# Kernel optimization log

Hardware: AMD Instinct MI355X
Metric: run time of the kernel (lower is better)

The kernel has to match this reference:

```python
import jax, jax.numpy as jnp
import numpy as np

D = 256      # hidden_dim / d_model
NH = 8       # num_heads
HD = D // NH # head_dim = 32
FF = 2048    # dim_feedforward
L = 2        # num_transformer_layers
CIN = 512
NC = 80      # num_classes
NA = 3       # num_anchors
EPS = 1e-5


def _ln(x, s, b):
    m = jnp.mean(x, axis=-1, keepdims=True)
    v = jnp.mean(jnp.square(x - m), axis=-1, keepdims=True)
    return (x - m) * jax.lax.rsqrt(v + EPS) * s + b


def setup_inputs() -> dict:
    key = jax.random.key(0)
    ks = iter(jax.random.split(key, 64))
    def g(shape, scale=0.02):
        return (jax.random.normal(next(ks), shape, dtype=jnp.float32) * scale)
    inp = {
        "x": jax.random.normal(next(ks), (4, CIN, 40, 40), dtype=jnp.float32),
        "conv_w": g((CIN, D)), "conv_b": jnp.zeros((D,), jnp.float32),
        "pos": jax.random.normal(next(ks), (1, D, 1, 1), dtype=jnp.float32),
        # stacked per-layer params [L, ...], weights stored as [in, out]
        "qw": g((L, D, D)), "qb": jnp.zeros((L, D)),
        "kw": g((L, D, D)), "kb": jnp.zeros((L, D)),
        "vw": g((L, D, D)), "vb": jnp.zeros((L, D)),
        "pw": g((L, D, D)), "pb": jnp.zeros((L, D)),
        "ln1s": jnp.ones((L, D)), "ln1b": jnp.zeros((L, D)),
        "ln2s": jnp.ones((L, D)), "ln2b": jnp.zeros((L, D)),
        "f1w": g((L, D, FF)), "f1b": jnp.zeros((L, FF)),
        "f2w": g((L, FF, D)), "f2b": jnp.zeros((L, D)),
        "cls_w1": g((D, D)), "cls_b1": jnp.zeros((D,)),
        "cls_w2": g((D, NA * NC)), "cls_b2": jnp.zeros((NA * NC,)),
        "box_w1": g((D, D)), "box_b1": jnp.zeros((D,)),
        "box_w2": g((D, NA * 4)), "box_b2": jnp.zeros((NA * 4,)),
        "obj_w1": g((D, D)), "obj_b1": jnp.zeros((D,)),
        "obj_w2": g((D, NA)), "obj_b2": jnp.zeros((NA,)),
    }
    return inp


def reference(x, conv_w, conv_b, pos, qw, qb, kw, kb, vw, vb, pw, pb,
              ln1s, ln1b, ln2s, ln2b, f1w, f1b, f2w, f2b,
              cls_w1, cls_b1, cls_w2, cls_b2,
              box_w1, box_b1, box_w2, box_b2,
              obj_w1, obj_b1, obj_w2, obj_b2):
    B, C, H, W = x.shape
    # 1x1 conv projection + positional encoding (broadcast scalar-per-channel)
    h = jnp.einsum('bchw,cd->bdhw', x, conv_w) + conv_b[None, :, None, None]
    h = h + pos  # broadcasts over B,H,W
    # flatten to sequence [B, N, D]
    N = H * W
    h = jnp.transpose(h.reshape(B, D, N), (0, 2, 1))

    scale = 1.0 / np.sqrt(HD)
    for i in range(L):
        # pre-norm MHSA
        y = _ln(h, ln1s[i], ln1b[i])
        q = (y @ qw[i] + qb[i]).reshape(B, N, NH, HD)
        k = (y @ kw[i] + kb[i]).reshape(B, N, NH, HD)
        v = (y @ vw[i] + vb[i]).reshape(B, N, NH, HD)
        scores = jnp.einsum('bnhd,bmhd->bhnm', q, k) * scale
        attn = jax.nn.softmax(scores, axis=-1)
        o = jnp.einsum('bhnm,bmhd->bnhd', attn, v).reshape(B, N, D)
        h = h + (o @ pw[i] + pb[i])
        # pre-norm FFN
        y = _ln(h, ln2s[i], ln2b[i])
        h = h + (jax.nn.relu(y @ f1w[i] + f1b[i]) @ f2w[i] + f2b[i])

    # prediction heads
    cls = jax.nn.relu(h @ cls_w1 + cls_b1) @ cls_w2 + cls_b2   # [B,N,NA*NC]
    box = jax.nn.relu(h @ box_w1 + box_b1) @ box_w2 + box_b2   # [B,N,NA*4]
    obj = jax.nn.relu(h @ obj_w1 + obj_b1) @ obj_w2 + obj_b2   # [B,N,NA]

    cls = jnp.transpose(cls.reshape(B, H, W, NA, NC), (0, 3, 1, 2, 4))
    box = jnp.transpose(box.reshape(B, H, W, NA, 4), (0, 3, 1, 2, 4))
    obj = jnp.transpose(obj.reshape(B, H, W, NA), (0, 3, 1, 2))
    return cls, box, obj
```

## Files before the change

kernel.cpp:

```cpp
#include <hip/hip_runtime.h>
#include <math.h>

#define BB   4
#define CIN  512
#define DD   256
#define NP   1600
#define TT   (BB*NP)
#define FF   2048
#define NHH  8
#define HDD  32
#define NA   3
#define NC   80

typedef __attribute__((ext_vector_type(8))) short bf16x8_t;
typedef __attribute__((ext_vector_type(4))) float f32x4_t;
typedef __attribute__((ext_vector_type(16))) float f32x16_t;

static __device__ __forceinline__ ushort f2bf(float f) {
    unsigned int u = __float_as_uint(f);
    u += 0x7FFF + ((u >> 16) & 1);
    return (ushort)(u >> 16);
}
static __device__ __forceinline__ float bf2f(ushort u) {
    return __uint_as_float((unsigned int)u << 16);
}
static __device__ __forceinline__ unsigned int cvt_pk_bf16(float lo, float hi) {
    unsigned int r;
    asm("v_cvt_pk_bf16_f32 %0, %1, %2" : "=v"(r) : "v"(lo), "v"(hi));
    return r;
}
static __device__ __forceinline__ void swap32(unsigned int& a, unsigned int& b) {
    asm("v_permlane32_swap_b32 %0, %1" : "+v"(a), "+v"(b));
}
static __device__ __forceinline__ bf16x8_t pack4(unsigned int a, unsigned int b,
                                                 unsigned int c, unsigned int d) {
    union { uint4 u; bf16x8_t v; } t;
    t.u = make_uint4(a, b, c, d);
    return t.v;
}

struct WDesc { const float* src; ushort* dst; int R; int C; int ntiles; float scale; };
struct WPrep { WDesc d[16]; };

__global__ __launch_bounds__(256) void wprep_kernel(WPrep p) {
    __shared__ float tile[32][33];
    int t = blockIdx.x;
    int i = 0;
    while (t >= p.d[i].ntiles) { t -= p.d[i].ntiles; i++; }
    const float* src = p.d[i].src;
    ushort* dst = p.d[i].dst;
    int R = p.d[i].R, C = p.d[i].C;
    float sc = p.d[i].scale;
    int tC = C >> 5;
    int r0 = (t / tC) * 32, c0 = (t % tC) * 32;
    int tx = threadIdx.x, ty = threadIdx.y;
    #pragma unroll
    for (int j = 0; j < 32; j += 8)
        tile[ty + j][tx] = src[(size_t)(r0 + ty + j) * C + (c0 + tx)];
    __syncthreads();
    #pragma unroll
    for (int j = 0; j < 32; j += 8)
        dst[(size_t)(c0 + ty + j) * R + (r0 + tx)] = f2bf(tile[tx][ty + j] * sc);
}

__global__ __launch_bounds__(256) void head2_wprep_kernel(
        const float* __restrict__ cls_w2, const float* __restrict__ box_w2,
        const float* __restrict__ obj_w2, ushort* __restrict__ dst)
{
    int nrow = blockIdx.x;
    int k = threadIdx.x;
    float v = 0.f;
    if (nrow < 240)                      v = cls_w2[k * 240 + nrow];
    else if (nrow >= 256 && nrow < 268)  v = box_w2[k * 12 + (nrow - 256)];
    else if (nrow >= 320 && nrow < 323)  v = obj_w2[k * 3 + (nrow - 320)];
    dst[(size_t)nrow * 256 + k] = f2bf(v);
}

__global__ void transpose_x_kernel(const float* __restrict__ x, ushort* __restrict__ xT) {
    __shared__ float tile[32][33];
    int b  = blockIdx.z;
    int c0 = blockIdx.x * 32;
    int n0 = blockIdx.y * 32;
    int tx = threadIdx.x, ty = threadIdx.y;
    #pragma unroll
    for (int j = 0; j < 32; j += 8) {
        tile[ty + j][tx] = x[b * CIN * NP + (c0 + ty + j) * NP + (n0 + tx)];
    }
    __syncthreads();
    #pragma unroll
    for (int j = 0; j < 32; j += 8) {
        xT[(size_t)(b * NP + n0 + ty + j) * CIN + (c0 + tx)] = f2bf(tile[tx][ty + j]);
    }
}

#define GEMM_CORE_LDA(A_, Bt_, K_, LDA_)                                         \
    __shared__ ushort As[64][72];                                                \
    __shared__ ushort Bs[64][72];                                                \
    int tid  = threadIdx.x;                                                      \
    int lane = tid & 63, wid = tid >> 6;                                         \
    int wm = wid >> 1, wn = wid & 1;                                             \
    int m0 = blockIdx.y * 64, n0 = blockIdx.x * 64;                              \
    int ln31 = lane & 31, lg = lane >> 5;                                        \
    int srow = tid >> 2;                                                         \
    int scol = (tid & 3) * 16;                                                   \
    const ushort* ag = (A_)  + (size_t)(m0 + srow) * (LDA_) + scol;              \
    const ushort* bg = (Bt_) + (size_t)(n0 + srow) * (K_) + scol;                \
    f32x16_t acc = {};                                                           \
    for (int k0 = 0; k0 < (K_); k0 += 64) {                                      \
        uint4 av0 = *(const uint4*)(ag + k0);                                    \
        uint4 av1 = *(const uint4*)(ag + k0 + 8);                                \
        uint4 bv0 = *(const uint4*)(bg + k0);                                    \
        uint4 bv1 = *(const uint4*)(bg + k0 + 8);                                \
        *(uint4*)&As[srow][scol]     = av0;                                      \
        *(uint4*)&As[srow][scol + 8] = av1;                                      \
        *(uint4*)&Bs[srow][scol]     = bv0;                                      \
        *(uint4*)&Bs[srow][scol + 8] = bv1;                                      \
        __syncthreads();                                                         \
        _Pragma("unroll")                                                        \
        for (int kc = 0; kc < 4; kc++) {                                         \
            bf16x8_t af = *(const bf16x8_t*)&As[wm * 32 + ln31][kc * 16 + lg * 8]; \
            bf16x8_t bf = *(const bf16x8_t*)&Bs[wn * 32 + ln31][kc * 16 + lg * 8]; \
            acc = __builtin_amdgcn_mfma_f32_32x32x16_bf16(af, bf, acc, 0, 0, 0); \
        }                                                                        \
        __syncthreads();                                                         \
    }                                                                            \
    int n = n0 + wn * 32 + ln31;

#define GEMM_CORE(A_, Bt_, K_) GEMM_CORE_LDA(A_, Bt_, K_, K_)

__global__ __launch_bounds__(256) void gemm_mfma_kernel(
        const ushort* __restrict__ A, const ushort* __restrict__ Bt,
        const float* __restrict__ bias, const float* __restrict__ bias2,
        const float* __restrict__ residual, float* __restrict__ Cf,
        ushort* __restrict__ Cbf, int M, int N, int K, int do_relu)
{
    GEMM_CORE(A, Bt, K)
    float bsum = bias[n] + (bias2 ? bias2[n] : 0.f);
    #pragma unroll
    for (int r = 0; r < 16; r++) {
        int row = (r & 3) + 8 * (r >> 2) + 4 * lg;
        int m = m0 + wm * 32 + row;
        float v = acc[r] + bsum;
        if (do_relu) v = fmaxf(v, 0.f);
        if (residual) v += residual[(size_t)m * N + n];
        if (Cf)  Cf [(size_t)m * N + n] = v;
        if (Cbf) Cbf[(size_t)m * N + n] = f2bf(v);
    }
}

__global__ __launch_bounds__(256) void gemm_qkv_kernel(
        const ushort* __restrict__ A, const ushort* __restrict__ Bt,
        const float* __restrict__ qb, const float* __restrict__ kb,
        const float* __restrict__ vb, ushort* __restrict__ q_out,
        ushort* __restrict__ k_out, ushort* __restrict__ vt_out, float qscale)
{
    GEMM_CORE(A, Bt, DD)
    int seg = n >> 8;
    int c   = n & 255;
    if (seg == 0) {
        float bsum = qb[c] * qscale;
        #pragma unroll
        for (int r = 0; r < 16; r++) {
            int row = (r & 3) + 8 * (r >> 2) + 4 * lg;
            q_out[(size_t)(m0 + wm * 32 + row) * DD + c] = f2bf(acc[r] + bsum);
        }
    } else if (seg == 1) {
        float bsum = kb[c];
        #pragma unroll
        for (int r = 0; r < 16; r++) {
            int row = (r & 3) + 8 * (r >> 2) + 4 * lg;
            k_out[(size_t)(m0 + wm * 32 + row) * DD + c] = f2bf(acc[r] + bsum);
        }
    } else {
        float bsum = vb[c];
        int b = m0 / NP;
        int nn0 = m0 - b * NP + wm * 32 + 4 * lg;
        int hh = c >> 5, d = c & 31;
        ushort* vt = vt_out + ((size_t)(b * NHH + hh) * HDD + d) * NP + nn0;
        #pragma unroll
        for (int qq = 0; qq < 4; qq++) {
            ushort4 w4 = make_ushort4(f2bf(acc[qq * 4 + 0] + bsum), f2bf(acc[qq * 4 + 1] + bsum),
                                      f2bf(acc[qq * 4 + 2] + bsum), f2bf(acc[qq * 4 + 3] + bsum));
            *(ushort4*)(vt + 8 * qq) = w4;
        }
    }
}

__global__ __launch_bounds__(256) void gemm_head1_kernel(
        const ushort* __restrict__ A, const ushort* __restrict__ Bt,
        const float* __restrict__ b0, const float* __restrict__ b1,
        const float* __restrict__ b2, ushort* __restrict__ t1)
{
    GEMM_CORE(A, Bt, DD)
    int seg = n >> 8;
    int c   = n & 255;
    float bsum = (seg == 0) ? b0[c] : (seg == 1) ? b1[c] : b2[c];
    #pragma unroll
    for (int r = 0; r < 16; r++) {
        int row = (r & 3) + 8 * (r >> 2) + 4 * lg;
        float v = fmaxf(acc[r] + bsum, 0.f);
        t1[(size_t)(m0 + wm * 32 + row) * 768 + n] = f2bf(v);
    }
}

__global__ __launch_bounds__(256) void gemm_head2_kernel(
        const ushort* __restrict__ t1, const ushort* __restrict__ Bt,
        const float* __restrict__ cb, const float* __restrict__ bb,
        const float* __restrict__ ob, float* __restrict__ cls_out,
        float* __restrict__ box_out, float* __restrict__ obj_out)
{
    int n0_ = blockIdx.x * 64;
    int seg_ = (n0_ >= 320) ? 2 : (n0_ >= 256) ? 1 : 0;
    const ushort* Aseg = t1 + seg_ * 256;
    GEMM_CORE_LDA(Aseg, Bt, 256, 768)

    float bsum = 0.f;
    float* outp = nullptr;
    int a_ = 0, s_ = 0, S_ = 1;
    if (seg_ == 0) {
        if (n < 240) { bsum = cb[n]; a_ = n / 80; s_ = n - a_ * 80; outp = cls_out; S_ = 80; }
    } else if (seg_ == 1) {
        int c = n - 256;
        if (c < 12) { bsum = bb[c]; a_ = c >> 2; s_ = c & 3; outp = box_out; S_ = 4; }
    } else {
        int c = n - 320;
        if (c < 3) { bsum = ob[c]; a_ = c; s_ = 0; outp = obj_out; S_ = 1; }
    }
    if (outp) {
        #pragma unroll
        for (int r = 0; r < 16; r++) {
            int row = (r & 3) + 8 * (r >> 2) + 4 * lg;
            int m = m0 + wm * 32 + row;
            int b = m / NP, hw = m - b * NP;
            outp[((size_t)(b * NA + a_) * NP + hw) * S_ + s_] = acc[r] + bsum;
        }
    }
}

__global__ __launch_bounds__(256) void ln_kernel(
        const float* __restrict__ x, const float* __restrict__ s,
        const float* __restrict__ b, ushort* __restrict__ y)
{
    int row = blockIdx.x;
    int t = threadIdx.x;
    float v = x[(size_t)row * DD + t];
    float s1 = v, s2 = v * v;
    #pragma unroll
    for (int m = 32; m >= 1; m >>= 1) {
        s1 += __shfl_xor(s1, m, 64);
        s2 += __shfl_xor(s2, m, 64);
    }
    __shared__ float w1[4], w2[4];
    int lane = t & 63, wid = t >> 6;
    if (lane == 0) { w1[wid] = s1; w2[wid] = s2; }
    __syncthreads();
    float S1 = w1[0] + w1[1] + w1[2] + w1[3];
    float S2 = w2[0] + w2[1] + w2[2] + w2[3];
    float mean = S1 * (1.f / DD);
    float var  = S2 * (1.f / DD) - mean * mean;
    float inv  = rsqrtf(var + 1e-5f);
    y[(size_t)row * DD + t] = f2bf((v - mean) * inv * s[t] + b[t]);
}

__global__ __launch_bounds__(320) void attn_mfma_kernel(
        const ushort* __restrict__ q, const ushort* __restrict__ k,
        const ushort* __restrict__ vt, ushort* __restrict__ o)
{
    __shared__ float mrg[5][64][36];
    int lane = threadIdx.x & 63;
    int wid  = threadIdx.x >> 6;
    int qq   = lane & 31;
    int hi   = lane >> 5;
    int h = blockIdx.y, b = blockIdx.z;
    int q0 = blockIdx.x * 64;
    int ks = wid * 320;

    const size_t tq = (size_t)(b * NP + q0 + qq) * DD + h * HDD;
    bf16x8_t qfA1 = *(const bf16x8_t*)(q + tq + hi * 8);
    bf16x8_t qfA2 = *(const bf16x8_t*)(q + tq + 16 + hi * 8);
    bf16x8_t qfB1 = *(const bf16x8_t*)(q + tq + (size_t)32 * DD + hi * 8);
    bf16x8_t qfB2 = *(const bf16x8_t*)(q + tq + (size_t)32 * DD + 16 + hi * 8);

    const ushort* kp = k + (size_t)(b * NP + qq) * DD + h * HDD + hi * 8;
    const ushort* vp = vt + ((size_t)(b * NHH + h) * HDD + qq) * NP + hi * 8;

    float lsumA = 0.f, lsumB = 0.f;
    f32x16_t otA = {};
    f32x16_t otB = {};

    bf16x8_t kf1 = *(const bf16x8_t*)(kp + (size_t)ks * DD);
    bf16x8_t kf2 = *(const bf16x8_t*)(kp + (size_t)ks * DD + 16);
    bf16x8_t vf1 = *(const bf16x8_t*)(vp + ks);
    bf16x8_t vf2 = *(const bf16x8_t*)(vp + ks + 16);

    for (int it = 0; it < 10; it++) {
        int kn = (it < 9) ? (ks + (it + 1) * 32) : ks;
        bf16x8_t nkf1 = *(const bf16x8_t*)(kp + (size_t)kn * DD);
        bf16x8_t nkf2 = *(const bf16x8_t*)(kp + (size_t)kn * DD + 16);
        bf16x8_t nvf1 = *(const bf16x8_t*)(vp + kn);
        bf16x8_t nvf2 = *(const bf16x8_t*)(vp + kn + 16);

        f32x16_t z = {};
        f32x16_t sA = __builtin_amdgcn_mfma_f32_32x32x16_bf16(kf1, qfA1, z, 0, 0, 0);
        sA = __builtin_amdgcn_mfma_f32_32x32x16_bf16(kf2, qfA2, sA, 0, 0, 0);
        f32x16_t sB = __builtin_amdgcn_mfma_f32_32x32x16_bf16(kf1, qfB1, z, 0, 0, 0);
        sB = __builtin_amdgcn_mfma_f32_32x32x16_bf16(kf2, qfB2, sB, 0, 0, 0);

        float pA[16], pB[16];
        #pragma unroll
        for (int r = 0; r < 16; r++) pA[r] = __builtin_amdgcn_exp2f(sA[r]);
        #pragma unroll
        for (int r = 0; r < 16; r++) pB[r] = __builtin_amdgcn_exp2f(sB[r]);
        lsumA += (((pA[0] + pA[1]) + (pA[2] + pA[3])) + ((pA[4] + pA[5]) + (pA[6] + pA[7])))
               + (((pA[8] + pA[9]) + (pA[10] + pA[11])) + ((pA[12] + pA[13]) + (pA[14] + pA[15])));
        lsumB += (((pB[0] + pB[1]) + (pB[2] + pB[3])) + ((pB[4] + pB[5]) + (pB[6] + pB[7])))
               + (((pB[8] + pB[9]) + (pB[10] + pB[11])) + ((pB[12] + pB[13]) + (pB[14] + pB[15])));

        unsigned int a0 = cvt_pk_bf16(pA[0],  pA[1]);
        unsigned int a1 = cvt_pk_bf16(pA[2],  pA[3]);
        unsigned int a2 = cvt_pk_bf16(pA[4],  pA[5]);
        unsigned int a3 = cvt_pk_bf16(pA[6],  pA[7]);
        unsigned int a4 = cvt_pk_bf16(pA[8],  pA[9]);
        unsigned int a5 = cvt_pk_bf16(pA[10], pA[11]);
        unsigned int a6 = cvt_pk_bf16(pA[12], pA[13]);
        unsigned int a7 = cvt_pk_bf16(pA[14], pA[15]);
        swap32(a2, a0); swap32(a3, a1); swap32(a6, a4); swap32(a7, a5);
        bf16x8_t pfA1 = pack4(a0, a1, a2, a3);
        bf16x8_t pfA2 = pack4(a4, a5, a6, a7);

        unsigned int b0 = cvt_pk_bf16(pB[0],  pB[1]);
        unsigned int b1 = cvt_pk_bf16(pB[2],  pB[3]);
        unsigned int b2 = cvt_pk_bf16(pB[4],  pB[5]);
        unsigned int b3 = cvt_pk_bf16(pB[6],  pB[7]);
        unsigned int b4 = cvt_pk_bf16(pB[8],  pB[9]);
        unsigned int b5 = cvt_pk_bf16(pB[10], pB[11]);
        unsigned int b6 = cvt_pk_bf16(pB[12], pB[13]);
        unsigned int b7 = cvt_pk_bf16(pB[14], pB[15]);
        swap32(b2, b0); swap32(b3, b1); swap32(b6, b4); swap32(b7, b5);
        bf16x8_t pfB1 = pack4(b0, b1, b2, b3);
        bf16x8_t pfB2 = pack4(b4, b5, b6, b7);

        otA = __builtin_amdgcn_mfma_f32_32x32x16_bf16(vf1, pfA1, otA, 0, 0, 0);
        otB = __builtin_amdgcn_mfma_f32_32x32x16_bf16(vf1, pfB1, otB, 0, 0, 0);
        otA = __builtin_amdgcn_mfma_f32_32x32x16_bf16(vf2, pfA2, otA, 0, 0, 0);
        otB = __builtin_amdgcn_mfma_f32_32x32x16_bf16(vf2, pfB2, otB, 0, 0, 0);

        kf1 = nkf1; kf2 = nkf2; vf1 = nvf1; vf2 = nvf2;
    }

    lsumA += __shfl_xor(lsumA, 32, 64);
    lsumB += __shfl_xor(lsumB, 32, 64);

    #pragma unroll
    for (int r = 0; r < 16; r++) mrg[wid][lane][r] = otA[r];
    mrg[wid][lane][16] = lsumA;
    #pragma unroll
    for (int r = 0; r < 16; r++) mrg[wid][lane][18 + r] = otB[r];
    mrg[wid][lane][34] = lsumB;
    __syncthreads();

    if (wid < 2) {
        int off = wid * 18;
        float ov[16] = {};
        float L = 0.f;
        #pragma unroll
        for (int w = 0; w < 5; w++) {
            #pragma unroll
            for (int r = 0; r < 16; r++) ov[r] += mrg[w][lane][off + r];
            L += mrg[w][lane][off + 16];
        }
        float inv = 1.f / L;
        size_t tqo = tq + (size_t)wid * 32 * DD;
        #pragma unroll
        for (int i = 0; i < 4; i++) {
            ushort4 s4 = make_ushort4(f2bf(ov[4 * i + 0] * inv), f2bf(ov[4 * i + 1] * inv),
                                      f2bf(ov[4 * i + 2] * inv), f2bf(ov[4 * i + 3] * inv));
            *(ushort4*)(o + tqo + 8 * i + 4 * hi) = s4;
        }
    }
}

static inline void launch_gemm(const ushort* A, const ushort* Bt, const float* bias,
                               const float* bias2, const float* res, float* Cf,
                               ushort* Cbf, int M, int N, int K, int relu,
                               hipStream_t s) {
    dim3 g(N / 64, M / 64), b(256);
    hipLaunchKernelGGL(gemm_mfma_kernel, g, b, 0, s,
                       A, Bt, bias, bias2, res, Cf, Cbf, M, N, K, relu);
}

extern "C" void kernel_launch(void* const* d_in, const int* in_sizes, int n_in,
                              void* d_out, int out_size, void* d_ws, size_t ws_size,
                              hipStream_t stream) {
    const float* x      = (const float*)d_in[0];
    const float* conv_w = (const float*)d_in[1];
    const float* conv_b = (const float*)d_in[2];
    const float* pos    = (const float*)d_in[3];
    const float* qw     = (const float*)d_in[4];
    const float* qb     = (const float*)d_in[5];
    const float* kw     = (const float*)d_in[6];
    const float* kb     = (const float*)d_in[7];
    const float* vw     = (const float*)d_in[8];
    const float* vb     = (const float*)d_in[9];
    const float* pw     = (const float*)d_in[10];
    const float* pb     = (const float*)d_in[11];
    const float* ln1s   = (const float*)d_in[12];
    const float* ln1b   = (const float*)d_in[13];
    const float* ln2s   = (const float*)d_in[14];
    const float* ln2b   = (const float*)d_in[15];
    const float* f1w    = (const float*)d_in[16];
    const float* f1b    = (const float*)d_in[17];
    const float* f2w    = (const float*)d_in[18];
    const float* f2b    = (const float*)d_in[19];
    const float* cls_w1 = (const float*)d_in[20];
    const float* cls_b1 = (const float*)d_in[21];
    const float* cls_w2 = (const float*)d_in[22];
    const float* cls_b2 = (const float*)d_in[23];
    const float* box_w1 = (const float*)d_in[24];
    const float* box_b1 = (const float*)d_in[25];
    const float* box_w2 = (const float*)d_in[26];
    const float* box_b2 = (const float*)d_in[27];
    const float* obj_w1 = (const float*)d_in[28];
    const float* obj_b1 = (const float*)d_in[29];
    const float* obj_w2 = (const float*)d_in[30];
    const float* obj_b2 = (const float*)d_in[31];

    float* out = (float*)d_out;
    const size_t TD = (size_t)TT * DD;

    char* p = (char*)d_ws;
    auto alloc = [&](size_t bytes) { char* r = p; p += (bytes + 255) & ~(size_t)255; return r; };
    float*  h    = (float*) alloc(TD * 4);
    ushort* y    = (ushort*)alloc(TD * 2);
    ushort* qB   = (ushort*)alloc(TD * 2);
    ushort* kB   = (ushort*)alloc(TD * 2);
    ushort* Vt   = (ushort*)alloc(TD * 2);
    ushort* oB   = (ushort*)alloc(TD * 2);
    ushort* hbf  = (ushort*)alloc(TD * 2);
    ushort* ffn  = (ushort*)alloc((size_t)TT * FF * 2);
    ushort* xT   = (ushort*)alloc((size_t)TT * CIN * 2);
    ushort* wT   = (ushort*)alloc((size_t)(2949120 + 98304) * 2);
    ushort* t1   = ffn;

    ushort* convT  = wT;
    ushort* qkvT   = wT + 131072;
    ushort* pwT    = wT + 524288;
    ushort* f1wT   = wT + 655360;
    ushort* f2wT   = wT + 1703936;
    ushort* headT  = wT + 2752512;
    ushort* head2T = wT + 2949120;

    const float QSCALE = 0.17677669529663687f * 1.4426950408889634f;

    WPrep wp;
    int total_tiles = 0;
    auto setd = [&](int i, const float* src, ushort* dst, int R, int C, float sc) {
        wp.d[i] = {src, dst, R, C, (R / 32) * (C / 32), sc};
        total_tiles += wp.d[i].ntiles;
    };
    setd(0,  conv_w, convT, CIN, DD, 1.f);
    setd(1,  qw,            qkvT,                    DD, DD, QSCALE);
    setd(2,  kw,            qkvT + 65536,            DD, DD, 1.f);
    setd(3,  vw,            qkvT + 131072,           DD, DD, 1.f);
    setd(4,  qw + DD * DD,  qkvT + 196608,           DD, DD, QSCALE);
    setd(5,  kw + DD * DD,  qkvT + 196608 + 65536,   DD, DD, 1.f);
    setd(6,  vw + DD * DD,  qkvT + 196608 + 131072,  DD, DD, 1.f);
    setd(7,  pw,            pwT,            DD, DD, 1.f);
    setd(8,  pw + DD * DD,  pwT + DD * DD,  DD, DD, 1.f);
    setd(9,  f1w,           f1wT,           DD, FF, 1.f);
    setd(10, f1w + DD * FF, f1wT + DD * FF, DD, FF, 1.f);
    setd(11, f2w,           f2wT,           FF, DD, 1.f);
    setd(12, f2w + FF * DD, f2wT + FF * DD, FF, DD, 1.f);
    setd(13, cls_w1, headT,          DD, DD, 1.f);
    setd(14, box_w1, headT + 65536,  DD, DD, 1.f);
    setd(15, obj_w1, headT + 131072, DD, DD, 1.f);
    hipLaunchKernelGGL(wprep_kernel, dim3(total_tiles), dim3(32, 8), 0, stream, wp);
    hipLaunchKernelGGL(head2_wprep_kernel, dim3(384), dim3(256), 0, stream,
                       cls_w2, box_w2, obj_w2, head2T);

    hipLaunchKernelGGL(transpose_x_kernel, dim3(CIN / 32, NP / 32, BB), dim3(32, 8),
                       0, stream, x, xT);

    launch_gemm(xT, convT, conv_b, pos, nullptr, h, nullptr, TT, DD, CIN, 0, stream);

    for (int i = 0; i < 2; i++) {
        hipLaunchKernelGGL(ln_kernel, dim3(TT), dim3(DD), 0, stream,
                           h, ln1s + i * DD, ln1b + i * DD, y);
        hipLaunchKernelGGL(gemm_qkv_kernel, dim3(768 / 64, TT / 64), dim3(256), 0, stream,
                           y, qkvT + (size_t)i * 196608, qb + i * DD, kb + i * DD,
                           vb + i * DD, qB, kB, Vt, QSCALE);

        hipLaunchKernelGGL(attn_mfma_kernel, dim3(NP / 64, NHH, BB), dim3(320), 0, stream,
                           qB, kB, Vt, oB);

        launch_gemm(oB, pwT + (size_t)i * DD * DD, pb + i * DD, nullptr, h, h, nullptr,
                    TT, DD, DD, 0, stream);

        hipLaunchKernelGGL(ln_kernel, dim3(TT), dim3(DD), 0, stream,
                           h, ln2s + i * DD, ln2b + i * DD, y);
        launch_gemm(y, f1wT + (size_t)i * DD * FF, f1b + i * FF, nullptr, nullptr,
                    nullptr, ffn, TT, FF, DD, 1, stream);
        launch_gemm(ffn, f2wT + (size_t)i * FF * DD, f2b + i * DD, nullptr, h,
                    (i == 0) ? h : nullptr, (i == 1) ? hbf : nullptr,
                    TT, DD, FF, 0, stream);
    }

    hipLaunchKernelGGL(gemm_head1_kernel, dim3(768 / 64, TT / 64), dim3(256), 0, stream,
                       hbf, headT, cls_b1, box_b1, obj_b1, t1);

    float* cls_out = out;
    float* box_out = out + (size_t)BB * NA * NP * NC;
    float* obj_out = box_out + (size_t)BB * NA * NP * 4;

    hipLaunchKernelGGL(gemm_head2_kernel, dim3(384 / 64, TT / 64), dim3(256), 0, stream,
                       t1, head2T, cls_b2, box_b2, obj_b2, cls_out, box_out, obj_out);
}
```

Baseline: 257.0 us.

## Fuse LayerNorm into QKV and FFN1 GEMM prologues

Removes the standalone LayerNorm kernels by computing row statistics and normalization inside the QKV and first FFN GEMM blocks. Each block normalizes its 64 rows of the fp32 residual into a full-K bf16 LDS tile, then streams only weight tiles. This avoids the intermediate bf16 activation buffer and four launches. In exchange, the LN work and the fp32 row reads are repeated for every column block, and the larger LDS footprint may lower occupancy.

```diff
diff --git a/kernel.cpp b/kernel.cpp
--- a/kernel.cpp
+++ b/kernel.cpp
@@ -128,6 +128,68 @@
 
 #define GEMM_CORE(A_, Bt_, K_) GEMM_CORE_LDA(A_, Bt_, K_, K_)
 
+#define GEMM_LN_CORE(HF_, Bt_, LNS_, LNB_)                                       \
+    __shared__ ushort Asf[64][264];                                              \
+    __shared__ ushort Bs[64][72];                                                \
+    __shared__ float red1[64][4];                                                \
+    __shared__ float red2[64][4];                                                \
+    int tid  = threadIdx.x;                                                      \
+    int lane = tid & 63, wid = tid >> 6;                                         \
+    int wm = wid >> 1, wn = wid & 1;                                             \
+    int m0 = blockIdx.y * 64, n0 = blockIdx.x * 64;                              \
+    int ln31 = lane & 31, lg = lane >> 5;                                        \
+    int srow = tid >> 2;                                                         \
+    int scol = (tid & 3) * 16;                                                   \
+    {                                                                            \
+        int r = tid >> 2, qd = tid & 3;                                          \
+        const float* hrow = (HF_) + (size_t)(m0 + r) * DD + qd * 64;             \
+        float s1 = 0.f, s2 = 0.f;                                                \
+        _Pragma("unroll")                                                        \
+        for (int j = 0; j < 64; j += 4) {                                        \
+            float4 v = *(const float4*)(hrow + j);                               \
+            s1 += (v.x + v.y) + (v.z + v.w);                                     \
+            s2 += (v.x * v.x + v.y * v.y) + (v.z * v.z + v.w * v.w);             \
+        }                                                                        \
+        red1[r][qd] = s1; red2[r][qd] = s2;                                      \
+        __syncthreads();                                                         \
+        float S1 = (red1[r][0] + red1[r][1]) + (red1[r][2] + red1[r][3]);        \
+        float S2 = (red2[r][0] + red2[r][1]) + (red2[r][2] + red2[r][3]);        \
+        float mean = S1 * (1.f / DD);                                            \
+        float var  = S2 * (1.f / DD) - mean * mean;                              \
+        float inv  = rsqrtf(var + 1e-5f);                                        \
+        _Pragma("unroll")                                                        \
+        for (int j = 0; j < 64; j += 4) {                                        \
+            float4 v  = *(const float4*)(hrow + j);                              \
+            int c = qd * 64 + j;                                                 \
+            float4 sv = *(const float4*)((LNS_) + c);                            \
+            float4 bv = *(const float4*)((LNB_) + c);                            \
+            ushort4 w;                                                           \
+            w.x = f2bf((v.x - mean) * inv * sv.x + bv.x);                        \
+            w.y = f2bf((v.y - mean) * inv * sv.y + bv.y);                        \
+            w.z = f2bf((v.z - mean) * inv * sv.z + bv.z);                        \
+            w.w = f2bf((v.w - mean) * inv * sv.w + bv.w);                        \
+            *(ushort4*)&Asf[r][c] = w;                                           \
+        }                                                                        \
+    }                                                                            \
+    const ushort* bg = (Bt_) + (size_t)(n0 + srow) * DD + scol;                  \
+    f32x16_t acc = {};                                                           \
+    __syncthreads();                                                             \
+    for (int k0 = 0; k0 < DD; k0 += 64) {                                        \
+        uint4 bv0 = *(const uint4*)(bg + k0);                                    \
+        uint4 bv1 = *(const uint4*)(bg + k0 + 8);                                \
+        *(uint4*)&Bs[srow][scol]     = bv0;                                      \
+        *(uint4*)&Bs[srow][scol + 8] = bv1;                                      \
+        __syncthreads();                                                         \
+        _Pragma("unroll")                                                        \
+        for (int kc = 0; kc < 4; kc++) {                                         \
+            bf16x8_t af = *(const bf16x8_t*)&Asf[wm * 32 + ln31][k0 + kc * 16 + lg * 8]; \
+            bf16x8_t bf = *(const bf16x8_t*)&Bs[wn * 32 + ln31][kc * 16 + lg * 8];       \
+            acc = __builtin_amdgcn_mfma_f32_32x32x16_bf16(af, bf, acc, 0, 0, 0); \
+        }                                                                        \
+        __syncthreads();                                                         \
+    }                                                                            \
+    int n = n0 + wn * 32 + ln31;
+
 __global__ __launch_bounds__(256) void gemm_mfma_kernel(
         const ushort* __restrict__ A, const ushort* __restrict__ Bt,
         const float* __restrict__ bias, const float* __restrict__ bias2,
@@ -148,13 +210,14 @@
     }
 }
 
-__global__ __launch_bounds__(256) void gemm_qkv_kernel(
-        const ushort* __restrict__ A, const ushort* __restrict__ Bt,
+__global__ __launch_bounds__(256) void gemm_ln_qkv_kernel(
+        const float* __restrict__ hf, const ushort* __restrict__ Bt,
+        const float* __restrict__ lns, const float* __restrict__ lnb,
         const float* __restrict__ qb, const float* __restrict__ kb,
         const float* __restrict__ vb, ushort* __restrict__ q_out,
         ushort* __restrict__ k_out, ushort* __restrict__ vt_out, float qscale)
 {
-    GEMM_CORE(A, Bt, DD)
+    GEMM_LN_CORE(hf, Bt, lns, lnb)
     int seg = n >> 8;
     int c   = n & 255;
     if (seg == 0) {
@@ -183,6 +246,21 @@
                                       f2bf(acc[qq * 4 + 2] + bsum), f2bf(acc[qq * 4 + 3] + bsum));
             *(ushort4*)(vt + 8 * qq) = w4;
         }
+    }
+}
+
+__global__ __launch_bounds__(256) void gemm_ln_ffn1_kernel(
+        const float* __restrict__ hf, const ushort* __restrict__ Bt,
+        const float* __restrict__ lns, const float* __restrict__ lnb,
+        const float* __restrict__ bias, ushort* __restrict__ Cbf)
+{
+    GEMM_LN_CORE(hf, Bt, lns, lnb)
+    float bsum = bias[n];
+    #pragma unroll
+    for (int r = 0; r < 16; r++) {
+        int row = (r & 3) + 8 * (r >> 2) + 4 * lg;
+        float v = fmaxf(acc[r] + bsum, 0.f);
+        Cbf[(size_t)(m0 + wm * 32 + row) * FF + n] = f2bf(v);
     }
 }
 
@@ -235,31 +313,6 @@
             outp[((size_t)(b * NA + a_) * NP + hw) * S_ + s_] = acc[r] + bsum;
         }
     }
-}
-
-__global__ __launch_bounds__(256) void ln_kernel(
-        const float* __restrict__ x, const float* __restrict__ s,
-        const float* __restrict__ b, ushort* __restrict__ y)
-{
-    int row = blockIdx.x;
-    int t = threadIdx.x;
-    float v = x[(size_t)row * DD + t];
-    float s1 = v, s2 = v * v;
-    #pragma unroll
-    for (int m = 32; m >= 1; m >>= 1) {
-        s1 += __shfl_xor(s1, m, 64);
-        s2 += __shfl_xor(s2, m, 64);
-    }
-    __shared__ float w1[4], w2[4];
-    int lane = t & 63, wid = t >> 6;
-    if (lane == 0) { w1[wid] = s1; w2[wid] = s2; }
-    __syncthreads();
-    float S1 = w1[0] + w1[1] + w1[2] + w1[3];
-    float S2 = w2[0] + w2[1] + w2[2] + w2[3];
-    float mean = S1 * (1.f / DD);
-    float var  = S2 * (1.f / DD) - mean * mean;
-    float inv  = rsqrtf(var + 1e-5f);
-    y[(size_t)row * DD + t] = f2bf((v - mean) * inv * s[t] + b[t]);
 }
 
 __global__ __launch_bounds__(320) void attn_mfma_kernel(
@@ -431,7 +484,6 @@
     char* p = (char*)d_ws;
     auto alloc = [&](size_t bytes) { char* r = p; p += (bytes + 255) & ~(size_t)255; return r; };
     float*  h    = (float*) alloc(TD * 4);
-    ushort* y    = (ushort*)alloc(TD * 2);
     ushort* qB   = (ushort*)alloc(TD * 2);
     ushort* kB   = (ushort*)alloc(TD * 2);
     ushort* Vt   = (ushort*)alloc(TD * 2);
@@ -484,11 +536,9 @@
     launch_gemm(xT, convT, conv_b, pos, nullptr, h, nullptr, TT, DD, CIN, 0, stream);
 
     for (int i = 0; i < 2; i++) {
-        hipLaunchKernelGGL(ln_kernel, dim3(TT), dim3(DD), 0, stream,
-                           h, ln1s + i * DD, ln1b + i * DD, y);
-        hipLaunchKernelGGL(gemm_qkv_kernel, dim3(768 / 64, TT / 64), dim3(256), 0, stream,
-                           y, qkvT + (size_t)i * 196608, qb + i * DD, kb + i * DD,
-                           vb + i * DD, qB, kB, Vt, QSCALE);
+        hipLaunchKernelGGL(gemm_ln_qkv_kernel, dim3(768 / 64, TT / 64), dim3(256), 0, stream,
+                           h, qkvT + (size_t)i * 196608, ln1s + i * DD, ln1b + i * DD,
+                           qb + i * DD, kb + i * DD, vb + i * DD, qB, kB, Vt, QSCALE);
 
         hipLaunchKernelGGL(attn_mfma_kernel, dim3(NP / 64, NHH, BB), dim3(320), 0, stream,
                            qB, kB, Vt, oB);
@@ -496,10 +546,10 @@
         launch_gemm(oB, pwT + (size_t)i * DD * DD, pb + i * DD, nullptr, h, h, nullptr,
                     TT, DD, DD, 0, stream);
 
-        hipLaunchKernelGGL(ln_kernel, dim3(TT), dim3(DD), 0, stream,
-                           h, ln2s + i * DD, ln2b + i * DD, y);
-        launch_gemm(y, f1wT + (size_t)i * DD * FF, f1b + i * FF, nullptr, nullptr,
-                    nullptr, ffn, TT, FF, DD, 1, stream);
+        hipLaunchKernelGGL(gemm_ln_ffn1_kernel, dim3(FF / 64, TT / 64), dim3(256), 0, stream,
+                           h, f1wT + (size_t)i * DD * FF, ln2s + i * DD, ln2b + i * DD,
+                           f1b + i * FF, ffn);
+
         launch_gemm(ffn, f2wT + (size_t)i * FF * DD, f2b + i * DD, nullptr, h,
                     (i == 0) ? h : nullptr, (i == 1) ? hbf : nullptr,
                     TT, DD, FF, 0, stream);
```

After: 490.7 us. +91.0%, slower.
